# Kernel tuning notes

Measured on AMD Instinct MI355X. Metric: run time of the kernel, lower is better.

## Reference

```python
import jax, jax.numpy as jnp
import numpy as np

# PM-field / module constants (from module source + plausible PMField defaults)
DT = 0.1          # PM-field integration step
EPS = 1e-4        # softening of gravitational flow
PM_STEPS = 4      # pm_steps
TAU = 0.9         # membrane_tau
M_GAIN = 0.1      # membrane_gain
EI_GAIN = 0.06    # VectorizedLateralEI gain
PLR = 0.001       # plasticity_lr (mu_lr = c_lr)


def setup_inputs() -> dict:
    key = jax.random.key(0)
    ks = jax.random.split(key, 8)
    B, D_IN, D_HID, D_LAT, N_C, CH, N_CLS = 16384, 784, 256, 8, 64, 64, 10
    x = jax.random.normal(ks[0], (B, D_IN), jnp.float32)
    W1 = jax.random.normal(ks[1], (D_IN, D_HID), jnp.float32) * 0.05
    b1 = jnp.zeros((D_HID,), jnp.float32)
    W2 = jax.random.normal(ks[2], (D_HID, D_LAT), jnp.float32) * 0.05
    b2 = jnp.zeros((D_LAT,), jnp.float32)
    mu = jax.random.uniform(ks[3], (N_C,), jnp.float32) * 0.5       # center strengths
    c = jax.random.normal(ks[4], (N_C, D_LAT), jnp.float32)         # center positions
    Wp = jax.random.normal(ks[5], (D_LAT, CH), jnp.float32) * 0.3
    bp = jnp.zeros((CH,), jnp.float32)
    Wr = jax.random.normal(ks[6], (CH, N_CLS), jnp.float32) * 0.1
    br = jnp.zeros((N_CLS,), jnp.float32)
    return {"x": x, "W1": W1, "b1": b1, "W2": W2, "b2": b2, "mu": mu,
            "c": c, "Wp": Wp, "bp": bp, "Wr": Wr, "br": br, "T": 5}


def _pm_evolve(z, mu, c):
    # Gravitational PM-field: z follows softened attraction to centers c with strengths mu.
    def body(z, _):
        d = c[None, :, :] - z[:, None, :]            # [B, N, D]
        r2 = jnp.sum(d * d, axis=-1) + EPS           # [B, N]
        z = z + DT * jnp.einsum('bn,bnd->bd', mu / r2, d)
        return z, None
    z, _ = jax.lax.scan(body, z, None, length=PM_STEPS)
    return z


def _forward(x, W1, b1, W2, b2, mu, c, Wp, bp, Wr, br, T):
    z = jnp.tanh(x @ W1 + b1) @ W2 + b2              # enc: [B, d_latent]
    h = jnp.zeros((x.shape[0], Wp.shape[1]), x.dtype)

    def step(carry, _):
        z, h, mu, c = carry
        z_ev = _pm_evolve(z, mu, c)
        h_proj = jnp.tanh(z_ev @ Wp + bp)
        h_new = TAU * h + M_GAIN * h_proj
        # lateral EI: excitation minus mean inhibition
        h_f = h_new + EI_GAIN * (h_new - jnp.mean(h_new, axis=-1, keepdims=True))
        logits = h_f @ Wr + br
        # vectorized Hebbian plasticity on PM centers (no-grad, like torch .data update)
        d = c[None, :, :] - z_ev[:, None, :]
        r2 = jnp.sum(d * d, axis=-1)                 # [B, N]
        act = jnp.exp(-r2)                           # center activity
        post = jnp.mean(h_f, axis=-1)                # postsynaptic drive [B]
        mu2 = mu + PLR * jnp.mean(act * post[:, None], axis=0)
        wsum = jnp.sum(act, axis=0)                  # [N]
        w = act / (wsum + EPS)[None, :]
        c2 = c + PLR * (jnp.einsum('bn,bd->nd', w, z_ev) - c * (wsum / (wsum + EPS))[:, None])
        mu2 = jax.lax.stop_gradient(mu2)
        c2 = jax.lax.stop_gradient(c2)
        return (z_ev, h_f, mu2, c2), logits

    (z, h, _, _), logits_seq = jax.lax.scan(step, (z, h, mu, c), None, length=T)
    return logits_seq[-1], z, h


def reference(x, W1, b1, W2, b2, mu, c, Wp, bp, Wr, br, T):
    return _forward(x, W1, b1, W2, b2, mu, c, Wp, bp, Wr, br, T)
```

## Files before the change

kernel.cpp:

```cpp
#include <hip/hip_runtime.h>
#include <math.h>

#define B_N     16384
#define D_IN    784
#define D_HID   256
#define D_LAT   8
#define N_CTR   64
#define CH_N    64
#define N_CLS   10

#define DT_C    0.1f
#define EPS_C   1e-4f
#define PM_STEPS 4
#define TAU_C   0.9f
#define MGAIN   0.1f
#define EIG     0.06f
#define PLR_C   0.001f
#define T_STEPS 5

#define KP      832

typedef short bf16x8 __attribute__((ext_vector_type(8)));
typedef float f32x4v __attribute__((ext_vector_type(4)));

__device__ __forceinline__ void split_pair(float a, float b, unsigned& hi, unsigned& lo) {
    unsigned ua = __float_as_uint(a), ub = __float_as_uint(b);
    hi = (ua >> 16) | (ub & 0xffff0000u);
    float ra = a - __uint_as_float(ua & 0xffff0000u);
    float rb = b - __uint_as_float(ub & 0xffff0000u);
    lo = (__float_as_uint(ra) >> 16) | (__float_as_uint(rb) & 0xffff0000u);
}

__global__ __launch_bounds__(256) void w1t_kernel(
    const float* __restrict__ W1, ushort* __restrict__ WtH, ushort* __restrict__ WtL)
{
    __shared__ float t[32][36];
    const int kb = blockIdx.x;
    const int nb = blockIdx.y;
    const int tid = threadIdx.x;
    {
        const int r = tid >> 3, c4 = (tid & 7) * 4;
        const int k = kb * 32 + r;
        float4 v = {0.f, 0.f, 0.f, 0.f};
        if (k < D_IN) v = *(const float4*)(W1 + (size_t)k * 256 + nb * 32 + c4);
        t[r][c4 + 0] = v.x; t[r][c4 + 1] = v.y; t[r][c4 + 2] = v.z; t[r][c4 + 3] = v.w;
    }
    __syncthreads();
    const int n = tid >> 3, kq = (tid & 7) * 4;
    float a0 = t[kq + 0][n], a1 = t[kq + 1][n], a2 = t[kq + 2][n], a3 = t[kq + 3][n];
    unsigned h0, l0, h1w, l1w;
    split_pair(a0, a1, h0, l0);
    split_pair(a2, a3, h1w, l1w);
    const size_t o = (size_t)(nb * 32 + n) * KP + kb * 32 + kq;
    uint2 hv; hv.x = h0; hv.y = h1w;
    uint2 lv; lv.x = l0; lv.y = l1w;
    *(uint2*)(WtH + o) = hv;
    *(uint2*)(WtL + o) = lv;
}

__global__ __launch_bounds__(256, 3) void enc1_kernel(
    const float* __restrict__ x, const ushort* __restrict__ WtH,
    const ushort* __restrict__ WtL, const float* __restrict__ b1,
    float* __restrict__ h1)
{
    __shared__ alignas(16) unsigned char AhiS[16384];
    __shared__ alignas(16) unsigned char AloS[16384];
    __shared__ alignas(16) unsigned char BhiS[8192];
    __shared__ alignas(16) unsigned char BloS[8192];

    const int tid = threadIdx.x;
    const int bx  = blockIdx.x;
    const int n0  = (bx & 3) * 64;
    const int m0  = (bx >> 2) * 128;

    const int m_s = tid >> 1, kh = tid & 1;
    const int n_s = tid >> 2, kq = tid & 3;
    const float*  xrow = x + (size_t)(m0 + m_s) * D_IN;
    const ushort* bhrow = WtH + (size_t)(n0 + n_s) * KP + kq * 16;
    const ushort* blrow = WtL + (size_t)(n0 + n_s) * KP + kq * 16;
    const unsigned offB0 = (unsigned)(n_s * 128) + (unsigned)(((2 * kq)     ^ (n_s & 7)) << 4);
    const unsigned offB1 = (unsigned)(n_s * 128) + (unsigned)(((2 * kq + 1) ^ (n_s & 7)) << 4);

    const int lane = tid & 63;
    const int wid  = tid >> 6;
    const int wm   = wid >> 1, wn = wid & 1;
    const int fr   = lane & 15, g = lane >> 4;
    const unsigned swz = (unsigned)((fr & 7) << 4);
    const int kgb  = g * 16;

    f32x4v acc[4][2];
    #pragma unroll
    for (int mi = 0; mi < 4; ++mi)
        #pragma unroll
        for (int ni = 0; ni < 2; ++ni) acc[mi][ni] = (f32x4v){0.f, 0.f, 0.f, 0.f};

    for (int kt = 0; kt < 13; ++kt) {
        const int kbase = kt * 64 + kh * 32;
        float4 av[8];
        #pragma unroll
        for (int q = 0; q < 8; ++q) {
            const int kk = kbase + q * 4;
            float4 z4 = {0.f, 0.f, 0.f, 0.f};
            av[q] = (kk < D_IN) ? *(const float4*)(xrow + kk) : z4;
        }
        #pragma unroll
        for (int q16 = 0; q16 < 4; ++q16) {
            uint4 hw, lw;
            split_pair(av[2 * q16].x,     av[2 * q16].y,     hw.x, lw.x);
            split_pair(av[2 * q16].z,     av[2 * q16].w,     hw.y, lw.y);
            split_pair(av[2 * q16 + 1].x, av[2 * q16 + 1].y, hw.z, lw.z);
            split_pair(av[2 * q16 + 1].z, av[2 * q16 + 1].w, hw.w, lw.w);
            const unsigned off = (unsigned)(m_s * 128) +
                (unsigned)((((kh * 4 + q16) ^ (m_s & 7))) << 4);
            *(uint4*)(AhiS + off) = hw;
            *(uint4*)(AloS + off) = lw;
        }
        {
            const int ko = kt * 64;
            uint4 h0 = *(const uint4*)(bhrow + ko);
            uint4 h1v = *(const uint4*)(bhrow + ko + 8);
            uint4 l0 = *(const uint4*)(blrow + ko);
            uint4 l1v = *(const uint4*)(blrow + ko + 8);
            *(uint4*)(BhiS + offB0) = h0;
            *(uint4*)(BhiS + offB1) = h1v;
            *(uint4*)(BloS + offB0) = l0;
            *(uint4*)(BloS + offB1) = l1v;
        }
        __syncthreads();

        #pragma unroll
        for (int ks = 0; ks < 2; ++ks) {
            const unsigned kb = (unsigned)(ks * 64 + kgb);
            bf16x8 ah[4], al[4];
            #pragma unroll
            for (int mi = 0; mi < 4; ++mi) {
                const unsigned off = (unsigned)((wm * 64 + mi * 16 + fr) * 128) + (kb ^ swz);
                ah[mi] = *(const bf16x8*)(AhiS + off);
                al[mi] = *(const bf16x8*)(AloS + off);
            }
            #pragma unroll
            for (int ni = 0; ni < 2; ++ni) {
                const unsigned offb = (unsigned)((wn * 32 + ni * 16 + fr) * 128) + (kb ^ swz);
                bf16x8 bh = *(const bf16x8*)(BhiS + offb);
                bf16x8 bl = *(const bf16x8*)(BloS + offb);
                #pragma unroll
                for (int mi = 0; mi < 4; ++mi) {
                    acc[mi][ni] = __builtin_amdgcn_mfma_f32_16x16x32_bf16(ah[mi], bh, acc[mi][ni], 0, 0, 0);
                    acc[mi][ni] = __builtin_amdgcn_mfma_f32_16x16x32_bf16(ah[mi], bl, acc[mi][ni], 0, 0, 0);
                    acc[mi][ni] = __builtin_amdgcn_mfma_f32_16x16x32_bf16(al[mi], bh, acc[mi][ni], 0, 0, 0);
                }
            }
        }
        __syncthreads();
    }

    #pragma unroll
    for (int ni = 0; ni < 2; ++ni) {
        const int col = n0 + wn * 32 + ni * 16 + fr;
        const float bias = b1[col];
        #pragma unroll
        for (int mi = 0; mi < 4; ++mi) {
            #pragma unroll
            for (int r = 0; r < 4; ++r) {
                const int row = m0 + wm * 64 + mi * 16 + g * 4 + r;
                h1[(size_t)row * 256 + col] = tanhf(acc[mi][ni][r] + bias);
            }
        }
    }
}

__global__ __launch_bounds__(256) void enc2_kernel(
    const float* __restrict__ h1, const float* __restrict__ W2,
    const float* __restrict__ b2, float* __restrict__ zT)
{
    __shared__ alignas(16) float hs[32][260];
    __shared__ alignas(16) float w2t[8][260];
    const int tid = threadIdx.x;
    const int r0 = blockIdx.x * 32;
    for (int i = tid; i < D_HID * D_LAT; i += 256) {
        int k = i >> 3, d = i & 7;
        w2t[d][k] = W2[i];
    }
    #pragma unroll
    for (int i = 0; i < 8; ++i) {
        int idx = tid + i * 256;
        int rr = idx >> 6, c4 = idx & 63;
        float4 v = *(const float4*)(h1 + (size_t)(r0 + rr) * D_HID + c4 * 4);
        *(float4*)&hs[rr][c4 * 4] = v;
    }
    __syncthreads();
    const int r = tid >> 3, d = tid & 7;
    float acc = 0.f;
    #pragma unroll 8
    for (int k4 = 0; k4 < 64; ++k4) {
        float4 a = *(const float4*)&hs[r][k4 * 4];
        float4 w = *(const float4*)&w2t[d][k4 * 4];
        acc = fmaf(a.x, w.x, acc);
        acc = fmaf(a.y, w.y, acc);
        acc = fmaf(a.z, w.z, acc);
        acc = fmaf(a.w, w.w, acc);
    }
    zT[(size_t)(r0 + r) * 8 + d] = acc + b2[d];
}

__global__ __launch_bounds__(256) void stepA2_kernel(
    float* __restrict__ zT, float* __restrict__ hT,
    const float* __restrict__ mu, const float* __restrict__ c,
    const float* __restrict__ Wp, const float* __restrict__ bp,
    const float* __restrict__ Wr, const float* __restrict__ br,
    float* __restrict__ part, float* __restrict__ out, int t)
{
    __shared__ alignas(16) float mu_s[64];
    __shared__ alignas(16) float c_s[512];
    __shared__ alignas(16) float wp_s[512];
    __shared__ alignas(16) float bp_s[64];
    __shared__ alignas(16) float wr_s[704];
    __shared__ alignas(16) float br_s[16];
    __shared__ alignas(16) float act_s[32 * 72];
    __shared__ alignas(16) float z_s[256];
    __shared__ alignas(16) float post_s[32];
    __shared__ alignas(16) float red2[4 * 64 * 10];
    const int tid = threadIdx.x;
    if (tid < 64) { mu_s[tid] = mu[tid]; bp_s[tid] = bp[tid]; }
    for (int i = tid; i < 512; i += 256) { c_s[i] = c[i]; wp_s[i] = Wp[i]; }
    const bool last = (t == T_STEPS - 1);
    if (last) {
        for (int i = tid; i < 640; i += 256) wr_s[(i / 10) * 11 + (i % 10)] = Wr[i];
        if (tid < N_CLS) br_s[tid] = br[tid];
    }
    __syncthreads();

    const int sub  = tid & 7;
    const int grp  = tid >> 3;
    const int b    = blockIdx.x * 32 + grp;
    const int lane = tid & 63;
    const int gbase = lane & ~7;

    float zown = zT[(size_t)b * 8 + sub];
    float z[8];
    #pragma unroll
    for (int d = 0; d < 8; ++d) z[d] = __shfl(zown, gbase + d, 64);

    #pragma unroll 1
    for (int it = 0; it < PM_STEPS; ++it) {
        float f[8];
        #pragma unroll
        for (int d = 0; d < 8; ++d) f[d] = 0.f;
        #pragma unroll
        for (int k = 0; k < 8; ++k) {
            const int n = sub + 8 * k;
            float dx[8];
            float r2 = EPS_C;
            #pragma unroll
            for (int d = 0; d < 8; ++d) {
                dx[d] = c_s[n * 8 + d] - z[d];
                r2 = fmaf(dx[d], dx[d], r2);
            }
            float w = mu_s[n] / r2;
            #pragma unroll
            for (int d = 0; d < 8; ++d) f[d] = fmaf(w, dx[d], f[d]);
        }
        #pragma unroll
        for (int m = 1; m <= 4; m <<= 1)
            #pragma unroll
            for (int d = 0; d < 8; ++d) f[d] += __shfl_xor(f[d], m, 64);
        #pragma unroll
        for (int d = 0; d < 8; ++d) z[d] = fmaf(DT_C, f[d], z[d]);
    }
    float zsel = z[0];
    #pragma unroll
    for (int d = 1; d < 8; ++d) if (sub == d) zsel = z[d];
    zT[(size_t)b * 8 + sub] = zsel;

    float hn[8];
    float s = 0.f;
    #pragma unroll
    for (int j = 0; j < 8; ++j) {
        const int ch = sub * 8 + j;
        float a = bp_s[ch];
        #pragma unroll
        for (int d = 0; d < 8; ++d) a = fmaf(z[d], wp_s[d * 64 + ch], a);
        hn[j] = tanhf(a);
    }
    if (t == 0) {
        #pragma unroll
        for (int j = 0; j < 8; ++j) { hn[j] = MGAIN * hn[j]; s += hn[j]; }
    } else {
        const float4* hp = (const float4*)(hT + (size_t)b * 64 + sub * 8);
        float4 h0 = hp[0], h1v = hp[1];
        hn[0] = TAU_C * h0.x + MGAIN * hn[0];
        hn[1] = TAU_C * h0.y + MGAIN * hn[1];
        hn[2] = TAU_C * h0.z + MGAIN * hn[2];
        hn[3] = TAU_C * h0.w + MGAIN * hn[3];
        hn[4] = TAU_C * h1v.x + MGAIN * hn[4];
        hn[5] = TAU_C * h1v.y + MGAIN * hn[5];
        hn[6] = TAU_C * h1v.z + MGAIN * hn[6];
        hn[7] = TAU_C * h1v.w + MGAIN * hn[7];
        #pragma unroll
        for (int j = 0; j < 8; ++j) s += hn[j];
    }
    #pragma unroll
    for (int m = 1; m <= 4; m <<= 1) s += __shfl_xor(s, m, 64);
    const float mean = s * (1.f / 64.f);
    float spost = 0.f;
    #pragma unroll
    for (int j = 0; j < 8; ++j) {
        hn[j] = hn[j] + EIG * (hn[j] - mean);
        spost += hn[j];
    }
    {
        float4 a0 = {hn[0], hn[1], hn[2], hn[3]};
        float4 a1 = {hn[4], hn[5], hn[6], hn[7]};
        float4* hp = (float4*)(hT + (size_t)b * 64 + sub * 8);
        hp[0] = a0; hp[1] = a1;
    }
    #pragma unroll
    for (int m = 1; m <= 4; m <<= 1) spost += __shfl_xor(spost, m, 64);

    if (!last) {
        z_s[tid] = zsel;
        if (sub == 0) post_s[grp] = spost * (1.f / 64.f);
        #pragma unroll
        for (int k = 0; k < 8; ++k) {
            const int n = sub + 8 * k;
            float r2 = 0.f;
            #pragma unroll
            for (int d = 0; d < 8; ++d) {
                float dd = c_s[n * 8 + d] - z[d];
                r2 = fmaf(dd, dd, r2);
            }
            act_s[grp * 72 + n] = expf(-r2);
        }
        __syncthreads();
        const int q = tid >> 6, n2 = tid & 63;
        float r[10];
        #pragma unroll
        for (int j = 0; j < 10; ++j) r[j] = 0.f;
        #pragma unroll
        for (int i = 0; i < 8; ++i) {
            const int g2 = q * 8 + i;
            float a = act_s[g2 * 72 + n2];
            r[0] += a;
            r[1] = fmaf(a, post_s[g2], r[1]);
            #pragma unroll
            for (int d = 0; d < 8; ++d)
                r[2 + d] = fmaf(a, z_s[g2 * 8 + d], r[2 + d]);
        }
        #pragma unroll
        for (int j = 0; j < 10; ++j) red2[(q * 64 + n2) * 10 + j] = r[j];
        __syncthreads();
        if (q == 0) {
            #pragma unroll
            for (int j = 0; j < 10; ++j) {
                float sv = (red2[(n2) * 10 + j] + red2[(64 + n2) * 10 + j]) +
                           (red2[(128 + n2) * 10 + j] + red2[(192 + n2) * 10 + j]);
                part[((size_t)blockIdx.x * 64 + n2) * 10 + j] = sv;
            }
        }
    } else {
        float lg[N_CLS];
        #pragma unroll
        for (int cls = 0; cls < N_CLS; ++cls) lg[cls] = 0.f;
        #pragma unroll
        for (int j = 0; j < 8; ++j) {
            const int ch = sub * 8 + j;
            #pragma unroll
            for (int cls = 0; cls < N_CLS; ++cls)
                lg[cls] = fmaf(hn[j], wr_s[ch * 11 + cls], lg[cls]);
        }
        #pragma unroll
        for (int m = 1; m <= 4; m <<= 1)
            #pragma unroll
            for (int cls = 0; cls < N_CLS; ++cls) lg[cls] += __shfl_xor(lg[cls], m, 64);
        if (sub == 0) {
            #pragma unroll
            for (int cls = 0; cls < N_CLS; ++cls)
                out[(size_t)b * 10 + cls] = lg[cls] + br_s[cls];
        }
        out[163840 + (size_t)b * 8 + sub] = zsel;
        {
            float4 a0 = {hn[0], hn[1], hn[2], hn[3]};
            float4 a1 = {hn[4], hn[5], hn[6], hn[7]};
            float4* op = (float4*)(out + 294912 + (size_t)b * 64 + sub * 8);
            op[0] = a0; op[1] = a1;
        }
    }
}

__global__ __launch_bounds__(256) void stepB2_kernel(
    const float* __restrict__ part,
    const float* __restrict__ mu_in, const float* __restrict__ c_in,
    float* __restrict__ mu_out, float* __restrict__ c_out)
{
    const int n = blockIdx.x, tid = threadIdx.x;
    __shared__ float red[256][10];
    const float* p0 = part + ((size_t)tid * 64 + n) * 10;
    const float* p1 = part + ((size_t)(tid + 256) * 64 + n) * 10;
    #pragma unroll
    for (int j = 0; j < 10; ++j) red[tid][j] = p0[j] + p1[j];
    __syncthreads();
    for (int s = 128; s > 0; s >>= 1) {
        if (tid < s) {
            #pragma unroll
            for (int j = 0; j < 10; ++j) red[tid][j] += red[tid + s][j];
        }
        __syncthreads();
    }
    if (tid == 0) {
        const float S1 = red[0][0];
        const float S2 = red[0][1] * (1.f / B_N);
        mu_out[n] = mu_in[n] + PLR_C * S2;
        const float denom = S1 + EPS_C;
        #pragma unroll
        for (int d = 0; d < 8; ++d) {
            float s3 = red[0][2 + d];
            c_out[n * 8 + d] = c_in[n * 8 + d] + PLR_C * (s3 / denom - c_in[n * 8 + d] * (S1 / denom));
        }
    }
}

extern "C" void kernel_launch(void* const* d_in, const int* in_sizes, int n_in,
                              void* d_out, int out_size, void* d_ws, size_t ws_size,
                              hipStream_t stream) {
    (void)in_sizes; (void)n_in; (void)out_size; (void)ws_size;
    const float* x   = (const float*)d_in[0];
    const float* W1  = (const float*)d_in[1];
    const float* b1  = (const float*)d_in[2];
    const float* W2  = (const float*)d_in[3];
    const float* b2  = (const float*)d_in[4];
    const float* mu0 = (const float*)d_in[5];
    const float* c0  = (const float*)d_in[6];
    const float* Wp  = (const float*)d_in[7];
    const float* bp  = (const float*)d_in[8];
    const float* Wr  = (const float*)d_in[9];
    const float* br  = (const float*)d_in[10];
    float* out = (float*)d_out;
    float* ws  = (float*)d_ws;

    float* h1    = ws;
    float* hT    = ws;
    float* part  = ws + 2113536;
    float* zT    = ws + 4194304;
    float* mu_buf = ws + 4325376;
    float* c_buf  = ws + 4325504;
    ushort* WtH  = (ushort*)(ws + 4326528);
    ushort* WtL  = (ushort*)(ws + 4433024);

    w1t_kernel<<<dim3(26, 8), 256, 0, stream>>>(W1, WtH, WtL);
    enc1_kernel<<<512, 256, 0, stream>>>(x, WtH, WtL, b1, h1);
    enc2_kernel<<<512, 256, 0, stream>>>(h1, W2, b2, zT);

    const float* mu_cur = mu0;
    const float* c_cur  = c0;
    for (int t = 0; t < T_STEPS; ++t) {
        stepA2_kernel<<<512, 256, 0, stream>>>(zT, hT, mu_cur, c_cur, Wp, bp, Wr, br,
                                               part, out, t);
        if (t < T_STEPS - 1) {
            float* mo = mu_buf + (t & 1) * 64;
            float* co = c_buf  + (t & 1) * 512;
            stepB2_kernel<<<64, 256, 0, stream>>>(part, mu_cur, c_cur, mo, co);
            mu_cur = mo;
            c_cur  = co;
        }
    }
}
```

Measured before the change: 141.9 us.

## Use fast math intrinsics, DPP reductions, and swizzled block order in encoder

Replaces the division, tanhf and expf in the PM step kernel with hardware reciprocal and fast exp approximations. Turns the first two xor-shuffle reduction stages into DPP quad-permute adds. Vectorizes the z_s reads in the plasticity reduction and remaps the encoder GEMM block index so that neighbouring blocks spread across tiles. This is meant to cut ALU and cross-lane latency in the small step kernels and improve cache locality in the GEMM, at the cost of slightly lower numerical accuracy.

```diff
diff --git a/kernel.cpp b/kernel.cpp
--- a/kernel.cpp
+++ b/kernel.cpp
@@ -30,6 +30,15 @@
     float rb = b - __uint_as_float(ub & 0xffff0000u);
     lo = (__float_as_uint(ra) >> 16) | (__float_as_uint(rb) & 0xffff0000u);
 }
+
+__device__ __forceinline__ float fast_rcp(float x) { return __builtin_amdgcn_rcpf(x); }
+__device__ __forceinline__ float fast_tanh(float a) {
+    float e = __expf(2.0f * a);
+    return 1.0f - 2.0f * fast_rcp(e + 1.0f);
+}
+
+#define DPP_XOR_ADD(v, CTRL) \
+    ((v) + __int_as_float(__builtin_amdgcn_update_dpp(0, __float_as_int(v), (CTRL), 0xF, 0xF, true)))
 
 __global__ __launch_bounds__(256) void w1t_kernel(
     const float* __restrict__ W1, ushort* __restrict__ WtH, ushort* __restrict__ WtL)
@@ -70,8 +79,9 @@
 
     const int tid = threadIdx.x;
     const int bx  = blockIdx.x;
-    const int n0  = (bx & 3) * 64;
-    const int m0  = (bx >> 2) * 128;
+    const int wk  = (bx & 7) * 64 + (bx >> 3);
+    const int n0  = (wk & 3) * 64;
+    const int m0  = (wk >> 2) * 128;
 
     const int m_s = tid >> 1, kh = tid & 1;
     const int n_s = tid >> 2, kq = tid & 3;
@@ -131,12 +141,12 @@
         #pragma unroll
         for (int ks = 0; ks < 2; ++ks) {
             const unsigned kb = (unsigned)(ks * 64 + kgb);
-            bf16x8 ah[4], al[4];
+            bf16x8 ahv[4], alv[4];
             #pragma unroll
             for (int mi = 0; mi < 4; ++mi) {
                 const unsigned off = (unsigned)((wm * 64 + mi * 16 + fr) * 128) + (kb ^ swz);
-                ah[mi] = *(const bf16x8*)(AhiS + off);
-                al[mi] = *(const bf16x8*)(AloS + off);
+                ahv[mi] = *(const bf16x8*)(AhiS + off);
+                alv[mi] = *(const bf16x8*)(AloS + off);
             }
             #pragma unroll
             for (int ni = 0; ni < 2; ++ni) {
@@ -145,9 +155,9 @@
                 bf16x8 bl = *(const bf16x8*)(BloS + offb);
                 #pragma unroll
                 for (int mi = 0; mi < 4; ++mi) {
-                    acc[mi][ni] = __builtin_amdgcn_mfma_f32_16x16x32_bf16(ah[mi], bh, acc[mi][ni], 0, 0, 0);
-                    acc[mi][ni] = __builtin_amdgcn_mfma_f32_16x16x32_bf16(ah[mi], bl, acc[mi][ni], 0, 0, 0);
-                    acc[mi][ni] = __builtin_amdgcn_mfma_f32_16x16x32_bf16(al[mi], bh, acc[mi][ni], 0, 0, 0);
+                    acc[mi][ni] = __builtin_amdgcn_mfma_f32_16x16x32_bf16(ahv[mi], bh, acc[mi][ni], 0, 0, 0);
+                    acc[mi][ni] = __builtin_amdgcn_mfma_f32_16x16x32_bf16(ahv[mi], bl, acc[mi][ni], 0, 0, 0);
+                    acc[mi][ni] = __builtin_amdgcn_mfma_f32_16x16x32_bf16(alv[mi], bh, acc[mi][ni], 0, 0, 0);
                 }
             }
         }
@@ -256,14 +266,16 @@
                 dx[d] = c_s[n * 8 + d] - z[d];
                 r2 = fmaf(dx[d], dx[d], r2);
             }
-            float w = mu_s[n] / r2;
-            #pragma unroll
-            for (int d = 0; d < 8; ++d) f[d] = fmaf(w, dx[d], f[d]);
-        }
-        #pragma unroll
-        for (int m = 1; m <= 4; m <<= 1)
-            #pragma unroll
-            for (int d = 0; d < 8; ++d) f[d] += __shfl_xor(f[d], m, 64);
+            float wgt = mu_s[n] * fast_rcp(r2);
+            #pragma unroll
+            for (int d = 0; d < 8; ++d) f[d] = fmaf(wgt, dx[d], f[d]);
+        }
+        #pragma unroll
+        for (int d = 0; d < 8; ++d) f[d] = DPP_XOR_ADD(f[d], 0xB1);
+        #pragma unroll
+        for (int d = 0; d < 8; ++d) f[d] = DPP_XOR_ADD(f[d], 0x4E);
+        #pragma unroll
+        for (int d = 0; d < 8; ++d) f[d] += __shfl_xor(f[d], 4, 64);
         #pragma unroll
         for (int d = 0; d < 8; ++d) z[d] = fmaf(DT_C, f[d], z[d]);
     }
@@ -280,7 +292,7 @@
         float a = bp_s[ch];
         #pragma unroll
         for (int d = 0; d < 8; ++d) a = fmaf(z[d], wp_s[d * 64 + ch], a);
-        hn[j] = tanhf(a);
+        hn[j] = fast_tanh(a);
     }
     if (t == 0) {
         #pragma unroll
@@ -299,8 +311,9 @@
         #pragma unroll
         for (int j = 0; j < 8; ++j) s += hn[j];
     }
-    #pragma unroll
-    for (int m = 1; m <= 4; m <<= 1) s += __shfl_xor(s, m, 64);
+    s = DPP_XOR_ADD(s, 0xB1);
+    s = DPP_XOR_ADD(s, 0x4E);
+    s += __shfl_xor(s, 4, 64);
     const float mean = s * (1.f / 64.f);
     float spost = 0.f;
     #pragma unroll
@@ -314,8 +327,9 @@
         float4* hp = (float4*)(hT + (size_t)b * 64 + sub * 8);
         hp[0] = a0; hp[1] = a1;
     }
-    #pragma unroll
-    for (int m = 1; m <= 4; m <<= 1) spost += __shfl_xor(spost, m, 64);
+    spost = DPP_XOR_ADD(spost, 0xB1);
+    spost = DPP_XOR_ADD(spost, 0x4E);
+    spost += __shfl_xor(spost, 4, 64);
 
     if (!last) {
         z_s[tid] = zsel;
@@ -329,7 +343,7 @@
                 float dd = c_s[n * 8 + d] - z[d];
                 r2 = fmaf(dd, dd, r2);
             }
-            act_s[grp * 72 + n] = expf(-r2);
+            act_s[grp * 72 + n] = __expf(-r2);
         }
         __syncthreads();
         const int q = tid >> 6, n2 = tid & 63;
@@ -340,11 +354,18 @@
         for (int i = 0; i < 8; ++i) {
             const int g2 = q * 8 + i;
             float a = act_s[g2 * 72 + n2];
+            const float4* zp = (const float4*)&z_s[g2 * 8];
+            float4 za = zp[0], zb = zp[1];
             r[0] += a;
             r[1] = fmaf(a, post_s[g2], r[1]);
-            #pragma unroll
-            for (int d = 0; d < 8; ++d)
-                r[2 + d] = fmaf(a, z_s[g2 * 8 + d], r[2 + d]);
+            r[2] = fmaf(a, za.x, r[2]);
+            r[3] = fmaf(a, za.y, r[3]);
+            r[4] = fmaf(a, za.z, r[4]);
+            r[5] = fmaf(a, za.w, r[5]);
+            r[6] = fmaf(a, zb.x, r[6]);
+            r[7] = fmaf(a, zb.y, r[7]);
+            r[8] = fmaf(a, zb.z, r[8]);
+            r[9] = fmaf(a, zb.w, r[9]);
         }
         #pragma unroll
         for (int j = 0; j < 10; ++j) red2[(q * 64 + n2) * 10 + j] = r[j];
@@ -369,9 +390,11 @@
                 lg[cls] = fmaf(hn[j], wr_s[ch * 11 + cls], lg[cls]);
         }
         #pragma unroll
-        for (int m = 1; m <= 4; m <<= 1)
-            #pragma unroll
-            for (int cls = 0; cls < N_CLS; ++cls) lg[cls] += __shfl_xor(lg[cls], m, 64);
+        for (int cls = 0; cls < N_CLS; ++cls) {
+            lg[cls] = DPP_XOR_ADD(lg[cls], 0xB1);
+            lg[cls] = DPP_XOR_ADD(lg[cls], 0x4E);
+            lg[cls] += __shfl_xor(lg[cls], 4, 64);
+        }
         if (sub == 0) {
             #pragma unroll
             for (int cls = 0; cls < N_CLS; ++cls)
```

After: 120.1 us. -15.4%, faster.
